# Kernel tuning notes

Measured on AMD Instinct MI355X. Metric: run time of the kernel, lower is better.

The kernel has to match this reference:

```python
import jax, jax.numpy as jnp
import numpy as np

D_MODEL = 256
N_LEVELS = 4
N_HEADS = 8
N_POINTS = 4
HEAD_DIM = D_MODEL // N_HEADS
SPATIAL_SHAPES = np.array([[128, 128], [64, 64], [32, 32], [16, 16]], dtype=np.int64)
LEN_IN = int((SPATIAL_SHAPES[:, 0] * SPATIAL_SHAPES[:, 1]).sum())  # 21760
BATCH = 2
LEN_Q = LEN_IN  # encoder self-attention


def setup_inputs() -> dict:
    key = jax.random.key(0)
    ks = jax.random.split(key, 12)
    C = D_MODEL
    lvl_start = np.concatenate([[0], np.cumsum(SPATIAL_SHAPES[:, 0] * SPATIAL_SHAPES[:, 1])[:-1]]).astype(np.int64)
    return {
        'query': jax.random.normal(ks[0], (BATCH, LEN_Q, C), jnp.float32),
        'reference_points': jax.random.uniform(ks[1], (BATCH, LEN_Q, N_LEVELS, 2), jnp.float32),
        'input_flatten': jax.random.normal(ks[2], (BATCH, LEN_IN, C), jnp.float32),
        'input_spatial_shapes': SPATIAL_SHAPES,          # static numpy: shapes must be concrete
        'input_level_start_index': lvl_start,            # static numpy
        'Wv': jax.random.normal(ks[3], (C, C), jnp.float32) / np.sqrt(C),
        'bv': jnp.zeros((C,), jnp.float32),
        'Woff': jax.random.normal(ks[4], (C, N_HEADS * N_LEVELS * N_POINTS * 2), jnp.float32) * 0.01,
        'boff': jax.random.normal(ks[5], (N_HEADS * N_LEVELS * N_POINTS * 2,), jnp.float32) * 0.5,
        'Wa': jax.random.normal(ks[6], (C, N_HEADS * N_LEVELS * N_POINTS), jnp.float32) * 0.01,
        'ba': jnp.zeros((N_HEADS * N_LEVELS * N_POINTS,), jnp.float32),
        'Wo': jax.random.normal(ks[7], (C, C), jnp.float32) / np.sqrt(C),
        'bo': jnp.zeros((C,), jnp.float32),
    }


def _grid_sample_bilinear(v, grid):
    """v: (B,H,W,D); grid: (B,Q,P,2) in [-1,1] (x,y). align_corners=False, zero padding."""
    B, H, W, D = v.shape
    x = (grid[..., 0] + 1.0) * 0.5 * W - 0.5
    y = (grid[..., 1] + 1.0) * 0.5 * H - 0.5
    x0 = jnp.floor(x)
    y0 = jnp.floor(y)
    wx = x - x0
    wy = y - y0
    b = jnp.arange(B)[:, None, None]

    def corner(xi, yi, w):
        valid = (xi >= 0) & (xi < W) & (yi >= 0) & (yi < H)
        xi_ = jnp.clip(xi, 0, W - 1).astype(jnp.int32)
        yi_ = jnp.clip(yi, 0, H - 1).astype(jnp.int32)
        return v[b, yi_, xi_] * (w * valid)[..., None]  # (B,Q,P,D)

    return (corner(x0, y0, (1 - wx) * (1 - wy))
            + corner(x0 + 1, y0, wx * (1 - wy))
            + corner(x0, y0 + 1, (1 - wx) * wy)
            + corner(x0 + 1, y0 + 1, wx * wy))


def _msdeform_attn(query, reference_points, input_flatten, spatial_shapes_np,
                   Wv, bv, Woff, boff, Wa, ba, Wo, bo):
    N, Lq, C = query.shape
    Lin = input_flatten.shape[1]
    M, L, P, D = N_HEADS, N_LEVELS, N_POINTS, HEAD_DIM

    value = (input_flatten @ Wv + bv).reshape(N, Lin, M, D)
    offsets = (query @ Woff + boff).reshape(N, Lq, M, L, P, 2)
    attn = jax.nn.softmax((query @ Wa + ba).reshape(N, Lq, M, L * P), axis=-1).reshape(N, Lq, M, L, P)

    # sampling locations in [0,1] -> grid in [-1,1]
    grids = 2.0 * (reference_points[:, :, None, :, None, :] + offsets) - 1.0  # (N,Lq,M,L,P,2)

    out = jnp.zeros((N * M, Lq, D), value.dtype)
    start = 0
    for lid in range(L):
        H_, W_ = int(spatial_shapes_np[lid, 0]), int(spatial_shapes_np[lid, 1])
        v_l = value[:, start:start + H_ * W_]                       # (N,HW,M,D)
        v_l = v_l.transpose(0, 2, 1, 3).reshape(N * M, H_, W_, D)   # (N*M,H,W,D)
        g_l = grids[:, :, :, lid].transpose(0, 2, 1, 3, 4).reshape(N * M, Lq, P, 2)
        sampled = _grid_sample_bilinear(v_l, g_l)                   # (N*M,Lq,P,D)
        a_l = attn[:, :, :, lid].transpose(0, 2, 1, 3).reshape(N * M, Lq, P)
        out = out + jnp.einsum('bqpd,bqp->bqd', sampled, a_l)
        start += H_ * W_

    out = out.reshape(N, M, Lq, D).transpose(0, 2, 1, 3).reshape(N, Lq, M * D)
    return out @ Wo + bo


def reference(query, reference_points, input_flatten, input_spatial_shapes,
              input_level_start_index, Wv, bv, Woff, boff, Wa, ba, Wo, bo):
    spatial_np = np.asarray(input_spatial_shapes)
    return _msdeform_attn(query, reference_points, input_flatten, spatial_np,
                          Wv, bv, Woff, boff, Wa, ba, Wo, bo)
```

## Files before the change

kernel.cpp:

```cpp
#include <hip/hip_runtime.h>
#include <cstdint>
#include <cstddef>

#define LEN_IN  21760
#define BATCH   2
#define MROWS   (BATCH * LEN_IN)

typedef short    sv8 __attribute__((ext_vector_type(8)));
typedef _Float16 hv8 __attribute__((ext_vector_type(8)));
typedef float    fv4 __attribute__((ext_vector_type(4)));

__device__ __forceinline__ unsigned short f2bf(float f) {
  unsigned u = __float_as_uint(f);
  u += 0x7fff + ((u >> 16) & 1);
  return (unsigned short)(u >> 16);
}
__device__ __forceinline__ float bf2f(unsigned short s) {
  return __uint_as_float(((unsigned)s) << 16);
}

__global__ __launch_bounds__(256) void cvt_weights(
    const float* __restrict__ Wv, const float* __restrict__ Woff,
    const float* __restrict__ Wa, const float* __restrict__ Wo,
    _Float16* __restrict__ WvT, short* __restrict__ WoffTh, short* __restrict__ WoffTl,
    _Float16* __restrict__ WaT, _Float16* __restrict__ WoT)
{
  const int b = blockIdx.x, k = threadIdx.x;
  if (b < 256) {
    WvT[(size_t)b * 256 + k] = (_Float16)Wv[(size_t)k * 256 + b];
  } else if (b < 512) {
    const int n = b - 256;
    const float v = Woff[(size_t)k * 256 + n];
    const unsigned short h = f2bf(v);
    WoffTh[(size_t)n * 256 + k] = h;
    WoffTl[(size_t)n * 256 + k] = f2bf(v - bf2f(h));
  } else if (b < 640) {
    const int n = b - 512;
    WaT[(size_t)n * 256 + k] = (_Float16)Wa[(size_t)k * 128 + n];
  } else {
    const int n = b - 640;
    WoT[(size_t)n * 256 + k] = (_Float16)Wo[(size_t)k * 256 + n];
  }
}

template<int TN, int AF32, int OUTMODE>
__global__ __launch_bounds__(256, 4) void gemm_f16t(
    const void* __restrict__ Ap, const _Float16* __restrict__ Bt,
    const float* __restrict__ bias, void* __restrict__ Cout)
{
  constexpr int JF = TN / 64;
  constexpr int NB = TN / 64;
  __shared__ _Float16 As[64 * 40];
  __shared__ _Float16 Bs[TN * 40];

  const int tid = threadIdx.x, lane = tid & 63, wave = tid >> 6;
  const int l15 = lane & 15, quad = lane >> 4;
  const int wc = wave * (TN / 4);
  const int rowBase = blockIdx.x * 64;
  const int rs = tid >> 2, ks = (tid & 3) * 8;

  float4 a32[2]; hv8 a16; hv8 bpf[NB];
  auto loadAB = [&](int k0) {
    if constexpr (AF32) {
      const float* A = (const float*)Ap;
      a32[0] = *(const float4*)&A[(size_t)(rowBase + rs) * 256 + k0 + ks];
      a32[1] = *(const float4*)&A[(size_t)(rowBase + rs) * 256 + k0 + ks + 4];
    } else {
      const _Float16* A = (const _Float16*)Ap;
      a16 = *(const hv8*)&A[(size_t)(rowBase + rs) * 256 + k0 + ks];
    }
#pragma unroll
    for (int p = 0; p < NB; ++p)
      bpf[p] = *(const hv8*)&Bt[(size_t)(p * 64 + rs) * 256 + k0 + ks];
  };

  loadAB(0);
  fv4 acc[4][JF] = {};

  for (int k0 = 0; k0 < 256; k0 += 32) {
    if (k0) __syncthreads();
    if constexpr (AF32) {
      const float fa[8] = {a32[0].x, a32[0].y, a32[0].z, a32[0].w,
                           a32[1].x, a32[1].y, a32[1].z, a32[1].w};
      hv8 h;
#pragma unroll
      for (int e = 0; e < 8; ++e) h[e] = (_Float16)fa[e];
      *(hv8*)&As[rs * 40 + ks] = h;
    } else {
      *(hv8*)&As[rs * 40 + ks] = a16;
    }
#pragma unroll
    for (int p = 0; p < NB; ++p) *(hv8*)&Bs[(p * 64 + rs) * 40 + ks] = bpf[p];
    __syncthreads();
    if (k0 < 224) loadAB(k0 + 32);

    hv8 af[4];
#pragma unroll
    for (int i = 0; i < 4; ++i)
      af[i] = *(const hv8*)&As[(i * 16 + l15) * 40 + quad * 8];
#pragma unroll
    for (int j = 0; j < JF; ++j) {
      const hv8 bf = *(const hv8*)&Bs[(wc + j * 16 + l15) * 40 + quad * 8];
#pragma unroll
      for (int i = 0; i < 4; ++i)
        acc[i][j] = __builtin_amdgcn_mfma_f32_16x16x32_f16(af[i], bf, acc[i][j], 0, 0, 0);
    }
  }

#pragma unroll
  for (int j = 0; j < JF; ++j) {
    const int col = wc + j * 16 + l15;
    const float bj = bias[col];
#pragma unroll
    for (int i = 0; i < 4; ++i)
#pragma unroll
      for (int rg = 0; rg < 4; ++rg) {
        const int row = rowBase + i * 16 + quad * 4 + rg;
        const float v = acc[i][j][rg] + bj;
        if constexpr (OUTMODE == 0) {
          ((float*)Cout)[(size_t)row * TN + col] = v;
        } else if constexpr (OUTMODE == 1) {
          ((_Float16*)Cout)[(size_t)row * TN + col] = (_Float16)v;
        } else {
          const int n = (row >= LEN_IN) ? 1 : 0;
          const int pix = row - n * LEN_IN;
          const int m = col >> 5, d = col & 31;
          ((_Float16*)Cout)[((size_t)(n * 8 + m) * LEN_IN + pix) * 32 + d] = (_Float16)v;
        }
      }
  }
}

__global__ __launch_bounds__(256, 3) void gemm_offs(
    const float* __restrict__ A, const short* __restrict__ Bth,
    const short* __restrict__ Btl, const float* __restrict__ boff,
    const float* __restrict__ refpts, float* __restrict__ C)
{
  __shared__ short Ash[64 * 40], Asl[64 * 40];
  __shared__ short Bsh[256 * 40], Bsl[256 * 40];

  const int tid = threadIdx.x, lane = tid & 63, wave = tid >> 6;
  const int l15 = lane & 15, quad = lane >> 4;
  const int wc = wave * 64;
  const int rowBase = blockIdx.x * 64;
  const int rs = tid >> 2, ks = (tid & 3) * 8;

  float4 a32[2]; sv8 bhp[4], blp[4];
  auto loadAB = [&](int k0) {
    a32[0] = *(const float4*)&A[(size_t)(rowBase + rs) * 256 + k0 + ks];
    a32[1] = *(const float4*)&A[(size_t)(rowBase + rs) * 256 + k0 + ks + 4];
#pragma unroll
    for (int p = 0; p < 4; ++p) {
      bhp[p] = *(const sv8*)&Bth[(size_t)(p * 64 + rs) * 256 + k0 + ks];
      blp[p] = *(const sv8*)&Btl[(size_t)(p * 64 + rs) * 256 + k0 + ks];
    }
  };

  loadAB(0);
  fv4 acc[4][4] = {};

  for (int k0 = 0; k0 < 256; k0 += 32) {
    if (k0) __syncthreads();
    {
      const float fa[8] = {a32[0].x, a32[0].y, a32[0].z, a32[0].w,
                           a32[1].x, a32[1].y, a32[1].z, a32[1].w};
      sv8 hh, ll;
#pragma unroll
      for (int e = 0; e < 8; ++e) {
        const unsigned short h = f2bf(fa[e]);
        hh[e] = (short)h;
        ll[e] = (short)f2bf(fa[e] - bf2f(h));
      }
      *(sv8*)&Ash[rs * 40 + ks] = hh;
      *(sv8*)&Asl[rs * 40 + ks] = ll;
    }
#pragma unroll
    for (int p = 0; p < 4; ++p) {
      *(sv8*)&Bsh[(p * 64 + rs) * 40 + ks] = bhp[p];
      *(sv8*)&Bsl[(p * 64 + rs) * 40 + ks] = blp[p];
    }
    __syncthreads();
    if (k0 < 224) loadAB(k0 + 32);

    sv8 ah[4], al[4];
#pragma unroll
    for (int i = 0; i < 4; ++i) {
      ah[i] = *(const sv8*)&Ash[(i * 16 + l15) * 40 + quad * 8];
      al[i] = *(const sv8*)&Asl[(i * 16 + l15) * 40 + quad * 8];
    }
#pragma unroll
    for (int j = 0; j < 4; ++j) {
      const sv8 bh = *(const sv8*)&Bsh[(wc + j * 16 + l15) * 40 + quad * 8];
      const sv8 bl = *(const sv8*)&Bsl[(wc + j * 16 + l15) * 40 + quad * 8];
#pragma unroll
      for (int i = 0; i < 4; ++i) {
        acc[i][j] = __builtin_amdgcn_mfma_f32_16x16x32_bf16(ah[i], bh, acc[i][j], 0, 0, 0);
        acc[i][j] = __builtin_amdgcn_mfma_f32_16x16x32_bf16(ah[i], bl, acc[i][j], 0, 0, 0);
        acc[i][j] = __builtin_amdgcn_mfma_f32_16x16x32_bf16(al[i], bh, acc[i][j], 0, 0, 0);
      }
    }
  }

#pragma unroll
  for (int j = 0; j < 4; ++j) {
    const int c = wc + j * 16 + l15;
    const int xy = c & 1, l = (c >> 3) & 3;
    const float Wl = (float)(128 >> l);
    const float bj = boff[c];
#pragma unroll
    for (int i = 0; i < 4; ++i)
#pragma unroll
      for (int rg = 0; rg < 4; ++rg) {
        const int row = rowBase + i * 16 + quad * 4 + rg;
        const float ref = refpts[(size_t)row * 8 + l * 2 + xy];
        C[(size_t)row * 256 + c] = (acc[i][j][rg] + bj + ref) * Wl - 0.5f;
      }
  }
}

__global__ __launch_bounds__(256, 6) void sample_kernel(
    const _Float16* __restrict__ value16,
    const float* __restrict__ coords,
    const _Float16* __restrict__ logits16,
    _Float16* __restrict__ outp16)
{
  __shared__ unsigned s_pair[4096];
  __shared__ float    s_attn[1024];

  const int tid = threadIdx.x;
  const int qBase = blockIdx.x * 8;

  if (tid < 64) {
    const hv8* lp = (const hv8*)&logits16[(size_t)(qBase + (tid >> 3)) * 128 + (tid & 7) * 16];
    const hv8 w0 = lp[0], w1 = lp[1];
    float w[16];
#pragma unroll
    for (int e = 0; e < 8; ++e) { w[e] = (float)w0[e]; w[8 + e] = (float)w1[e]; }
    float mx = w[0];
#pragma unroll
    for (int i = 1; i < 16; ++i) mx = fmaxf(mx, w[i]);
    float sum = 0.f;
#pragma unroll
    for (int i = 0; i < 16; ++i) { w[i] = expf(w[i] - mx); sum += w[i]; }
    const float inv = 1.f / sum;
#pragma unroll
    for (int p = 0; p < 16; ++p) s_attn[p * 64 + tid] = w[p] * inv;
  }
  __syncthreads();

#pragma unroll
  for (int k = 0; k < 4; ++k) {
    const int i = tid + 256 * k;
    const int p = i >> 6, q = (i >> 3) & 7, m = i & 7;
    const int l = p >> 2, pp = p & 3;
    const int qg = qBase + q;
    const float2 of = *(const float2*)&coords[(size_t)qg * 256 + ((m * 4 + l) * 4 + pp) * 2];
    const float aw = s_attn[i];
    const int W = 128 >> l;
    const int st = (l == 0) ? 0 : (l == 1) ? 16384 : (l == 2) ? 20480 : 21504;
    const float xf = floorf(of.x), yf = floorf(of.y);
    const int x0 = (int)xf, y0 = (int)yf;
    const float wx = of.x - xf, wy = of.y - yf;
    uint4 rec;
    unsigned* rp = &rec.x;
#pragma unroll
    for (int c = 0; c < 4; ++c) {
      const int dx = c & 1, dy = c >> 1;
      const int xi = x0 + dx, yi = y0 + dy;
      const bool valid = (xi >= 0) & (xi < W) & (yi >= 0) & (yi < W);
      const float w = (dx ? wx : 1.f - wx) * (dy ? wy : 1.f - wy) * aw;
      union { _Float16 h; unsigned short s; } pk;
      pk.h = (_Float16)w;
      const unsigned idx = (unsigned)(st + yi * W + xi);
      rp[c] = valid ? (idx | ((unsigned)pk.s << 16)) : 0u;
    }
    *(uint4*)&s_pair[i * 4] = rec;
  }
  __syncthreads();

  const int wave = tid >> 6, lane = tid & 63;
  const int qloc = wave * 2 + (lane >> 5);
  const int sub = lane & 31, m = sub >> 2, j = sub & 3;
  const int qg = qBase + qloc;
  const int n = (qg >= LEN_IN) ? 1 : 0;
  const char* base = (const char*)value16 + (size_t)(n * 8 + m) * LEN_IN * 64 + j * 16;
  const int lb = qloc * 8 + m;

  float acc8[8] = {0.f, 0.f, 0.f, 0.f, 0.f, 0.f, 0.f, 0.f};
#pragma unroll 4
  for (int p = 0; p < 16; ++p) {
    const uint4 u4 = *(const uint4*)&s_pair[(p * 64 + lb) * 4];
    const unsigned uu[4] = {u4.x, u4.y, u4.z, u4.w};
#pragma unroll
    for (int c = 0; c < 4; ++c) {
      const unsigned u = uu[c];
      union { unsigned short s; _Float16 h; } pk;
      pk.s = (unsigned short)(u >> 16);
      const float w = (float)pk.h;
      const hv8 v = *(const hv8*)(base + (size_t)(u & 32767u) * 64);
#pragma unroll
      for (int e = 0; e < 8; ++e) acc8[e] = fmaf(w, (float)v[e], acc8[e]);
    }
  }

  hv8 o;
#pragma unroll
  for (int e = 0; e < 8; ++e) o[e] = (_Float16)acc8[e];
  *(hv8*)&outp16[(size_t)qg * 256 + m * 32 + j * 8] = o;
}

extern "C" void kernel_launch(void* const* d_in, const int* in_sizes, int n_in,
                              void* d_out, int out_size, void* d_ws, size_t ws_size,
                              hipStream_t stream) {
  const float* query   = (const float*)d_in[0];
  const float* refpts  = (const float*)d_in[1];
  const float* flatten = (const float*)d_in[2];
  const float* Wv   = (const float*)d_in[5];
  const float* bv   = (const float*)d_in[6];
  const float* Woff = (const float*)d_in[7];
  const float* boff = (const float*)d_in[8];
  const float* Wa   = (const float*)d_in[9];
  const float* ba   = (const float*)d_in[10];
  const float* Wo   = (const float*)d_in[11];
  const float* bo   = (const float*)d_in[12];
  float* out = (float*)d_out;

  const size_t NE = (size_t)MROWS * 256;
  _Float16* value16  = (_Float16*)d_ws;
  float*    coords   = (float*)(value16 + NE);
  _Float16* logits16 = (_Float16*)(coords + NE);
  _Float16* outp16   = logits16 + NE / 2;
  _Float16* WvT16    = outp16 + NE;
  short*    WoffTh   = (short*)(WvT16 + 256 * 256);
  short*    WoffTl   = WoffTh + 256 * 256;
  _Float16* WaT16    = (_Float16*)(WoffTl + 256 * 256);
  _Float16* WoT16    = WaT16 + 128 * 256;

  const dim3 blk(256);
  const int mtiles = MROWS / 64;

  cvt_weights<<<dim3(896), blk, 0, stream>>>(Wv, Woff, Wa, Wo,
      WvT16, WoffTh, WoffTl, WaT16, WoT16);

  gemm_f16t<256, 1, 2><<<dim3(mtiles), blk, 0, stream>>>(flatten, WvT16, bv, value16);
  gemm_offs<<<dim3(mtiles), blk, 0, stream>>>(query, WoffTh, WoffTl, boff, refpts, coords);
  gemm_f16t<128, 1, 1><<<dim3(mtiles), blk, 0, stream>>>(query, WaT16, ba, logits16);
  sample_kernel<<<dim3(MROWS / 8), blk, 0, stream>>>(value16, coords, logits16, outp16);
  gemm_f16t<256, 0, 0><<<dim3(mtiles), blk, 0, stream>>>(outp16, WoT16, bo, out);
}
```

Measured before the change: 316.6 us.

## Pipeline GEMM loads with double-buffered LDS and switch offset GEMM to fp16 split

The main GEMMs now keep four A stages in registers and double-buffer A and B in shared memory. This leaves one raw barrier per K step instead of two `__syncthreads`, so global loads can overlap more with MFMA work. The offset GEMM replaces its bf16 hi/lo split with an fp16 hi/lo split, and the two halves of the split weight now sit in one buffer. The weight-conversion kernel becomes a 64x64 tiled transpose through shared memory. These changes add register and LDS pressure and drop the occupancy hints from the launch bounds. The fp16 split also changes rounding behaviour for small offset values.

After: 295.1 us. 6.8% less time.

```diff
diff --git a/kernel.cpp b/kernel.cpp
--- a/kernel.cpp
+++ b/kernel.cpp
@@ -6,52 +6,55 @@
 #define BATCH   2
 #define MROWS   (BATCH * LEN_IN)
 
-typedef short    sv8 __attribute__((ext_vector_type(8)));
 typedef _Float16 hv8 __attribute__((ext_vector_type(8)));
 typedef float    fv4 __attribute__((ext_vector_type(4)));
 
-__device__ __forceinline__ unsigned short f2bf(float f) {
-  unsigned u = __float_as_uint(f);
-  u += 0x7fff + ((u >> 16) & 1);
-  return (unsigned short)(u >> 16);
-}
-__device__ __forceinline__ float bf2f(unsigned short s) {
-  return __uint_as_float(((unsigned)s) << 16);
-}
+#define WAIT_LGKM0() __builtin_amdgcn_s_waitcnt(0xC07F)
+#define RAW_BARRIER() __builtin_amdgcn_s_barrier()
 
 __global__ __launch_bounds__(256) void cvt_weights(
     const float* __restrict__ Wv, const float* __restrict__ Woff,
     const float* __restrict__ Wa, const float* __restrict__ Wo,
-    _Float16* __restrict__ WvT, short* __restrict__ WoffTh, short* __restrict__ WoffTl,
+    _Float16* __restrict__ WvT, _Float16* __restrict__ WoffT2,
     _Float16* __restrict__ WaT, _Float16* __restrict__ WoT)
 {
-  const int b = blockIdx.x, k = threadIdx.x;
-  if (b < 256) {
-    WvT[(size_t)b * 256 + k] = (_Float16)Wv[(size_t)k * 256 + b];
-  } else if (b < 512) {
-    const int n = b - 256;
-    const float v = Woff[(size_t)k * 256 + n];
-    const unsigned short h = f2bf(v);
-    WoffTh[(size_t)n * 256 + k] = h;
-    WoffTl[(size_t)n * 256 + k] = f2bf(v - bf2f(h));
-  } else if (b < 640) {
-    const int n = b - 512;
-    WaT[(size_t)n * 256 + k] = (_Float16)Wa[(size_t)k * 128 + n];
-  } else {
-    const int n = b - 640;
-    WoT[(size_t)n * 256 + k] = (_Float16)Wo[(size_t)k * 256 + n];
+  __shared__ float t[64][65];
+  const int id = blockIdx.x, tid = threadIdx.x;
+  const int c = tid & 63, r4 = tid >> 6;
+
+  const float* src; _Float16* dst; int N; bool split = false; int nt, kt;
+  if (id < 16)      { src = Wv;   dst = WvT;    N = 256; nt = id & 3;        kt = id >> 2; }
+  else if (id < 32) { src = Woff; dst = WoffT2; N = 256; nt = (id - 16) & 3; kt = (id - 16) >> 2; split = true; }
+  else if (id < 40) { src = Wa;   dst = WaT;    N = 128; nt = (id - 32) & 1; kt = (id - 32) >> 1; }
+  else              { src = Wo;   dst = WoT;    N = 256; nt = (id - 40) & 3; kt = (id - 40) >> 2; }
+  const int nb = nt * 64, kb = kt * 64;
+
+#pragma unroll
+  for (int rr = 0; rr < 16; ++rr) {
+    const int r = rr * 4 + r4;
+    t[r][c] = src[(size_t)(kb + r) * N + nb + c];
+  }
+  __syncthreads();
+#pragma unroll
+  for (int rr = 0; rr < 16; ++rr) {
+    const int r = rr * 4 + r4;
+    const float v = t[c][r];
+    const _Float16 h = (_Float16)v;
+    dst[(size_t)(nb + r) * 256 + kb + c] = h;
+    if (split)
+      dst[(size_t)(256 + nb + r) * 256 + kb + c] = (_Float16)(v - (float)h);
   }
 }
 
 template<int TN, int AF32, int OUTMODE>
-__global__ __launch_bounds__(256, 4) void gemm_f16t(
+__global__ __launch_bounds__(256) void gemm_pipe(
     const void* __restrict__ Ap, const _Float16* __restrict__ Bt,
     const float* __restrict__ bias, void* __restrict__ Cout)
 {
+  constexpr int NB = TN / 64;
   constexpr int JF = TN / 64;
-  constexpr int NB = TN / 64;
-  __shared__ _Float16 As[64 * 40];
-  __shared__ _Float16 Bs[TN * 40];
+  __shared__ _Float16 As[2][64 * 40];
+  __shared__ _Float16 Bs[2][TN * 40];
 
   const int tid = threadIdx.x, lane = tid & 63, wave = tid >> 6;
   const int l15 = lane & 15, quad = lane >> 4;
@@ -59,48 +62,62 @@
   const int rowBase = blockIdx.x * 64;
   const int rs = tid >> 2, ks = (tid & 3) * 8;
 
-  float4 a32[2]; hv8 a16; hv8 bpf[NB];
-  auto loadAB = [&](int k0) {
+  const float*    A32 = (const float*)Ap;
+  const _Float16* A16 = (const _Float16*)Ap;
+
+  float4 pa[4][2];
+  hv8    pa16[4];
+  hv8    pb[NB];
+
+  auto issueA = [&](int it) {
+    const int k0 = it * 32, s = it & 3;
     if constexpr (AF32) {
-      const float* A = (const float*)Ap;
-      a32[0] = *(const float4*)&A[(size_t)(rowBase + rs) * 256 + k0 + ks];
-      a32[1] = *(const float4*)&A[(size_t)(rowBase + rs) * 256 + k0 + ks + 4];
+      pa[s][0] = *(const float4*)&A32[(size_t)(rowBase + rs) * 256 + k0 + ks];
+      pa[s][1] = *(const float4*)&A32[(size_t)(rowBase + rs) * 256 + k0 + ks + 4];
     } else {
-      const _Float16* A = (const _Float16*)Ap;
-      a16 = *(const hv8*)&A[(size_t)(rowBase + rs) * 256 + k0 + ks];
-    }
+      pa16[s] = *(const hv8*)&A16[(size_t)(rowBase + rs) * 256 + k0 + ks];
+    }
+  };
+  auto issueB = [&](int it) {
+    const int k0 = it * 32;
 #pragma unroll
     for (int p = 0; p < NB; ++p)
-      bpf[p] = *(const hv8*)&Bt[(size_t)(p * 64 + rs) * 256 + k0 + ks];
+      pb[p] = *(const hv8*)&Bt[(size_t)(p * 64 + rs) * 256 + k0 + ks];
   };
 
-  loadAB(0);
+  issueA(0); issueA(1); issueA(2); issueA(3);
+  issueB(0);
+
   fv4 acc[4][JF] = {};
 
-  for (int k0 = 0; k0 < 256; k0 += 32) {
-    if (k0) __syncthreads();
+#pragma unroll
+  for (int it = 0; it < 8; ++it) {
+    const int sa = it & 3, sb = it & 1;
     if constexpr (AF32) {
-      const float fa[8] = {a32[0].x, a32[0].y, a32[0].z, a32[0].w,
-                           a32[1].x, a32[1].y, a32[1].z, a32[1].w};
+      const float4 f0 = pa[sa][0], f1 = pa[sa][1];
+      const float fa[8] = {f0.x, f0.y, f0.z, f0.w, f1.x, f1.y, f1.z, f1.w};
       hv8 h;
 #pragma unroll
       for (int e = 0; e < 8; ++e) h[e] = (_Float16)fa[e];
-      *(hv8*)&As[rs * 40 + ks] = h;
+      *(hv8*)&As[sb][rs * 40 + ks] = h;
     } else {
-      *(hv8*)&As[rs * 40 + ks] = a16;
-    }
-#pragma unroll
-    for (int p = 0; p < NB; ++p) *(hv8*)&Bs[(p * 64 + rs) * 40 + ks] = bpf[p];
-    __syncthreads();
-    if (k0 < 224) loadAB(k0 + 32);
+      *(hv8*)&As[sb][rs * 40 + ks] = pa16[sa];
+    }
+#pragma unroll
+    for (int p = 0; p < NB; ++p)
+      *(hv8*)&Bs[sb][(p * 64 + rs) * 40 + ks] = pb[p];
+    if (it + 4 < 8) issueA(it + 4);
+    if (it + 1 < 8) issueB(it + 1);
+    WAIT_LGKM0();
+    RAW_BARRIER();
 
     hv8 af[4];
 #pragma unroll
     for (int i = 0; i < 4; ++i)
-      af[i] = *(const hv8*)&As[(i * 16 + l15) * 40 + quad * 8];
+      af[i] = *(const hv8*)&As[sb][(i * 16 + l15) * 40 + quad * 8];
 #pragma unroll
     for (int j = 0; j < JF; ++j) {
-      const hv8 bf = *(const hv8*)&Bs[(wc + j * 16 + l15) * 40 + quad * 8];
+      const hv8 bf = *(const hv8*)&Bs[sb][(wc + j * 16 + l15) * 40 + quad * 8];
 #pragma unroll
       for (int i = 0; i < 4; ++i)
         acc[i][j] = __builtin_amdgcn_mfma_f32_16x16x32_f16(af[i], bf, acc[i][j], 0, 0, 0);
@@ -131,13 +148,13 @@
   }
 }
 
-__global__ __launch_bounds__(256, 3) void gemm_offs(
-    const float* __restrict__ A, const short* __restrict__ Bth,
-    const short* __restrict__ Btl, const float* __restrict__ boff,
-    const float* __restrict__ refpts, float* __restrict__ C)
+__global__ __launch_bounds__(256) void gemm_offs_pipe(
+    const float* __restrict__ A, const _Float16* __restrict__ B2,
+    const float* __restrict__ boff, const float* __restrict__ refpts,
+    float* __restrict__ C)
 {
-  __shared__ short Ash[64 * 40], Asl[64 * 40];
-  __shared__ short Bsh[256 * 40], Bsl[256 * 40];
+  __shared__ _Float16 Ash[64 * 40], Asl[64 * 40];
+  __shared__ _Float16 Bs[512 * 40];
 
   const int tid = threadIdx.x, lane = tid & 63, wave = tid >> 6;
   const int l15 = lane & 15, quad = lane >> 4;
@@ -145,60 +162,68 @@
   const int rowBase = blockIdx.x * 64;
   const int rs = tid >> 2, ks = (tid & 3) * 8;
 
-  float4 a32[2]; sv8 bhp[4], blp[4];
-  auto loadAB = [&](int k0) {
-    a32[0] = *(const float4*)&A[(size_t)(rowBase + rs) * 256 + k0 + ks];
-    a32[1] = *(const float4*)&A[(size_t)(rowBase + rs) * 256 + k0 + ks + 4];
-#pragma unroll
-    for (int p = 0; p < 4; ++p) {
-      bhp[p] = *(const sv8*)&Bth[(size_t)(p * 64 + rs) * 256 + k0 + ks];
-      blp[p] = *(const sv8*)&Btl[(size_t)(p * 64 + rs) * 256 + k0 + ks];
-    }
+  float4 pa[4][2];
+  hv8 pb[8];
+
+  auto issueA = [&](int it) {
+    const int k0 = it * 32, s = it & 3;
+    pa[s][0] = *(const float4*)&A[(size_t)(rowBase + rs) * 256 + k0 + ks];
+    pa[s][1] = *(const float4*)&A[(size_t)(rowBase + rs) * 256 + k0 + ks + 4];
   };
-
-  loadAB(0);
+  auto issueB = [&](int it) {
+    const int k0 = it * 32;
+#pragma unroll
+    for (int p = 0; p < 8; ++p)
+      pb[p] = *(const hv8*)&B2[(size_t)(p * 64 + rs) * 256 + k0 + ks];
+  };
+
+  issueA(0); issueA(1); issueA(2); issueA(3);
+  issueB(0);
+
   fv4 acc[4][4] = {};
 
-  for (int k0 = 0; k0 < 256; k0 += 32) {
-    if (k0) __syncthreads();
+#pragma unroll
+  for (int it = 0; it < 8; ++it) {
+    const int sa = it & 3;
     {
-      const float fa[8] = {a32[0].x, a32[0].y, a32[0].z, a32[0].w,
-                           a32[1].x, a32[1].y, a32[1].z, a32[1].w};
-      sv8 hh, ll;
+      const float4 f0 = pa[sa][0], f1 = pa[sa][1];
+      const float fa[8] = {f0.x, f0.y, f0.z, f0.w, f1.x, f1.y, f1.z, f1.w};
+      hv8 hh, ll;
 #pragma unroll
       for (int e = 0; e < 8; ++e) {
-        const unsigned short h = f2bf(fa[e]);
-        hh[e] = (short)h;
-        ll[e] = (short)f2bf(fa[e] - bf2f(h));
+        hh[e] = (_Float16)fa[e];
+        ll[e] = (_Float16)(fa[e] - (float)hh[e]);
       }
-      *(sv8*)&Ash[rs * 40 + ks] = hh;
-      *(sv8*)&Asl[rs * 40 + ks] = ll;
-    }
-#pragma unroll
-    for (int p = 0; p < 4; ++p) {
-      *(sv8*)&Bsh[(p * 64 + rs) * 40 + ks] = bhp[p];
-      *(sv8*)&Bsl[(p * 64 + rs) * 40 + ks] = blp[p];
-    }
-    __syncthreads();
-    if (k0 < 224) loadAB(k0 + 32);
-
-    sv8 ah[4], al[4];
+      *(hv8*)&Ash[rs * 40 + ks] = hh;
+      *(hv8*)&Asl[rs * 40 + ks] = ll;
+    }
+#pragma unroll
+    for (int p = 0; p < 8; ++p)
+      *(hv8*)&Bs[(p * 64 + rs) * 40 + ks] = pb[p];
+    if (it + 4 < 8) issueA(it + 4);
+    if (it + 1 < 8) issueB(it + 1);
+    WAIT_LGKM0();
+    RAW_BARRIER();
+
+    hv8 ah[4], al[4];
 #pragma unroll
     for (int i = 0; i < 4; ++i) {
-      ah[i] = *(const sv8*)&Ash[(i * 16 + l15) * 40 + quad * 8];
-      al[i] = *(const sv8*)&Asl[(i * 16 + l15) * 40 + quad * 8];
+      ah[i] = *(const hv8*)&Ash[(i * 16 + l15) * 40 + quad * 8];
+      al[i] = *(const hv8*)&Asl[(i * 16 + l15) * 40 + quad * 8];
     }
 #pragma unroll
     for (int j = 0; j < 4; ++j) {
-      const sv8 bh = *(const sv8*)&Bsh[(wc + j * 16 + l15) * 40 + quad * 8];
-      const sv8 bl = *(const sv8*)&Bsl[(wc + j * 16 + l15) * 40 + quad * 8];
+      const hv8 bh = *(const hv8*)&Bs[(wc + j * 16 + l15) * 40 + quad * 8];
+      const hv8 bl = *(const hv8*)&Bs[((256 + wc + j * 16 + l15)) * 40 + quad * 8];
 #pragma unroll
       for (int i = 0; i < 4; ++i) {
-        acc[i][j] = __builtin_amdgcn_mfma_f32_16x16x32_bf16(ah[i], bh, acc[i][j], 0, 0, 0);
-        acc[i][j] = __builtin_amdgcn_mfma_f32_16x16x32_bf16(ah[i], bl, acc[i][j], 0, 0, 0);
-        acc[i][j] = __builtin_amdgcn_mfma_f32_16x16x32_bf16(al[i], bh, acc[i][j], 0, 0, 0);
+        acc[i][j] = __builtin_amdgcn_mfma_f32_16x16x32_f16(ah[i], bh, acc[i][j], 0, 0, 0);
+        acc[i][j] = __builtin_amdgcn_mfma_f32_16x16x32_f16(ah[i], bl, acc[i][j], 0, 0, 0);
+        acc[i][j] = __builtin_amdgcn_mfma_f32_16x16x32_f16(al[i], bh, acc[i][j], 0, 0, 0);
       }
     }
+    WAIT_LGKM0();
+    RAW_BARRIER();
   }
 
 #pragma unroll
@@ -330,21 +355,19 @@
   float*    coords   = (float*)(value16 + NE);
   _Float16* logits16 = (_Float16*)(coords + NE);
   _Float16* outp16   = logits16 + NE / 2;
-  _Float16* WvT16    = outp16 + NE;
-  short*    WoffTh   = (short*)(WvT16 + 256 * 256);
-  short*    WoffTl   = WoffTh + 256 * 256;
-  _Float16* WaT16    = (_Float16*)(WoffTl + 256 * 256);
-  _Float16* WoT16    = WaT16 + 128 * 256;
+  _Float16* WvT      = outp16 + NE;
+  _Float16* WoffT2   = WvT + 256 * 256;
+  _Float16* WaT      = WoffT2 + 512 * 256;
+  _Float16* WoT      = WaT + 128 * 256;
 
   const dim3 blk(256);
   const int mtiles = MROWS / 64;
 
-  cvt_weights<<<dim3(896), blk, 0, stream>>>(Wv, Woff, Wa, Wo,
-      WvT16, WoffTh, WoffTl, WaT16, WoT16);
-
-  gemm_f16t<256, 1, 2><<<dim3(mtiles), blk, 0, stream>>>(flatten, WvT16, bv, value16);
-  gemm_offs<<<dim3(mtiles), blk, 0, stream>>>(query, WoffTh, WoffTl, boff, refpts, coords);
-  gemm_f16t<128, 1, 1><<<dim3(mtiles), blk, 0, stream>>>(query, WaT16, ba, logits16);
+  cvt_weights<<<dim3(56), blk, 0, stream>>>(Wv, Woff, Wa, Wo, WvT, WoffT2, WaT, WoT);
+
+  gemm_pipe<256, 1, 2><<<dim3(mtiles), blk, 0, stream>>>(flatten, WvT, bv, value16);
+  gemm_offs_pipe<<<dim3(mtiles), blk, 0, stream>>>(query, WoffT2, boff, refpts, coords);
+  gemm_pipe<128, 1, 1><<<dim3(mtiles), blk, 0, stream>>>(query, WaT, ba, logits16);
   sample_kernel<<<dim3(MROWS / 8), blk, 0, stream>>>(value16, coords, logits16, outp16);
-  gemm_f16t<256, 0, 0><<<dim3(mtiles), blk, 0, stream>>>(outp16, WoT16, bo, out);
-}
+  gemm_pipe<256, 0, 0><<<dim3(mtiles), blk, 0, stream>>>(outp16, WoT, bo, out);
+}
```
